# Kernel optimization log

Hardware: AMD Instinct MI355X
Metric: run time of the kernel (lower is better)

The kernel has to match this reference:

```python
import jax, jax.numpy as jnp
import numpy as np

B, N, M = 2, 2048, 128
H, D = 16, 64
IN_DIM, CTX_DIM = 1024, 768


def layernorm(x, g, b, eps=1e-5):
    mu = x.mean(-1, keepdims=True)
    var = ((x - mu) ** 2).mean(-1, keepdims=True)
    return (x - mu) * jax.lax.rsqrt(var + eps) * g + b


def setup_inputs() -> dict:
    key = jax.random.key(0)
    ks = jax.random.split(key, 8)
    w = lambda i, sh: jax.random.normal(ks[i], sh, jnp.float32) * 0.02
    return {
        "x": jax.random.normal(ks[0], (B, N, IN_DIM), jnp.float32),
        "c_emb": jax.random.normal(ks[1], (B, M, CTX_DIM), jnp.float32),
        "ln_g": jnp.ones((IN_DIM,), jnp.float32),
        "ln_b": jnp.zeros((IN_DIM,), jnp.float32),
        "ctx_ln_g": jnp.ones((CTX_DIM,), jnp.float32),
        "ctx_ln_b": jnp.zeros((CTX_DIM,), jnp.float32),
        "W_ctx": w(2, (CTX_DIM, 2 * D)),
        "b_ctx": jnp.zeros((2 * D,), jnp.float32),
        "W_q": w(3, (IN_DIM, H * D)),
        "W_kv": w(4, (IN_DIM, 2 * H * D)),
        "null_kv": jax.random.normal(ks[5], (2, D), jnp.float32),
        "W_out": w(6, (H * D, IN_DIM)),
        "out_ln_g": jnp.ones((IN_DIM,), jnp.float32),
        "out_ln_b": jnp.zeros((IN_DIM,), jnp.float32),
    }


def reference(x, c_emb, ln_g, ln_b, ctx_ln_g, ctx_ln_b, W_ctx, b_ctx,
              W_q, W_kv, null_kv, W_out, out_ln_g, out_ln_b):
    b, n, _ = x.shape
    xn = layernorm(x, ln_g, ln_b)
    q = (xn @ W_q).reshape(b, n, H, D)                      # [b,n,h,d]
    kv = (xn @ W_kv).reshape(b, n, 2, H, D)
    k, v = kv[:, :, 0], kv[:, :, 1]                         # [b,n,h,d]
    # context projected to a single shared-across-heads k and v
    ckv = layernorm(c_emb, ctx_ln_g, ctx_ln_b) @ W_ctx + b_ctx
    ck, cv = jnp.split(ckv, 2, axis=-1)                     # [b,m,d]
    nk = jnp.broadcast_to(null_kv[0], (b, 1, D))
    nv = jnp.broadcast_to(null_kv[1], (b, 1, D))
    k_ext = jnp.concatenate([nk, ck], axis=1)               # [b,m+1,d]
    v_ext = jnp.concatenate([nv, cv], axis=1)
    scale = D ** -0.5
    s_self = jnp.einsum('bnhd,bkhd->bhnk', q, k) * scale    # [b,h,n,n]
    s_ctx = jnp.einsum('bnhd,bkd->bhnk', q, k_ext) * scale  # [b,h,n,m+1]
    w = jax.nn.softmax(jnp.concatenate([s_self, s_ctx], axis=-1), axis=-1)
    w_self, w_ctx = w[..., :n], w[..., n:]
    out = (jnp.einsum('bhnk,bkhd->bnhd', w_self, v)
           + jnp.einsum('bhnk,bkd->bnhd', w_ctx, v_ext))    # [b,n,h,d]
    out = out.reshape(b, n, H * D) @ W_out                  # [b,n,input_dim]
    return layernorm(out, out_ln_g, out_ln_b)
```

## Files before the change

### kernel.cpp

```cpp
#include <hip/hip_runtime.h>
#include <cstdint>
#include <cstddef>

typedef __attribute__((ext_vector_type(8))) short bf16x8;
typedef __attribute__((ext_vector_type(4))) short bf16x4;
typedef __attribute__((ext_vector_type(4))) float f32x4;
typedef __attribute__((ext_vector_type(4))) unsigned int u32x4;
typedef __attribute__((ext_vector_type(2))) unsigned int u32x2;

__device__ inline unsigned short f2b(float f){
  unsigned int u = __float_as_uint(f);
  u += 0x7fffu + ((u >> 16) & 1u);
  return (unsigned short)(u >> 16);
}
__device__ inline unsigned int pk2(float a, float b){
  unsigned int ua = __float_as_uint(a) + 0x8000u;
  unsigned int ub = __float_as_uint(b) + 0x8000u;
  return __builtin_amdgcn_perm(ub, ua, 0x07060302u);
}
__device__ inline void gl2lds16(const void* g, void* l){
  __builtin_amdgcn_global_load_lds(
      (const __attribute__((address_space(1))) unsigned int*)g,
      (__attribute__((address_space(3))) unsigned int*)l, 16, 0, 0);
}

#define QSCALE 0.18033688011112042f

__global__ __launch_bounds__(256) void wcvt_kernel(
    const float* __restrict__ Wq, const float* __restrict__ Wkv,
    const float* __restrict__ Wout,
    unsigned short* __restrict__ Wqkv_t, unsigned short* __restrict__ Wout_t)
{
  __shared__ short tile[64*72];
  int cg0 = blockIdx.x * 64;
  int kt  = blockIdx.y * 64;
  const float* src; int ld; int col0; unsigned short* dst; int drow0;
  if (cg0 < 1024)      { src = Wq;   ld = 1024; col0 = cg0;        dst = Wqkv_t; drow0 = cg0; }
  else if (cg0 < 3072) { src = Wkv;  ld = 2048; col0 = cg0 - 1024; dst = Wqkv_t; drow0 = cg0; }
  else                 { src = Wout; ld = 1024; col0 = cg0 - 3072; dst = Wout_t; drow0 = cg0 - 3072; }
  int t = threadIdx.x;
  #pragma unroll
  for (int i = 0; i < 16; ++i){
    int lin = t + 256*i;
    int k = lin >> 6, c = lin & 63;
    tile[k*72 + c] = (short)f2b(src[(size_t)(kt + k)*ld + col0 + c]);
  }
  __syncthreads();
  #pragma unroll
  for (int i = 0; i < 16; ++i){
    int lin = t + 256*i;
    int c = lin >> 6, k = lin & 63;
    dst[(size_t)(drow0 + c)*1024 + kt + k] = (unsigned short)tile[k*72 + c];
  }
}

template<bool BF16OUT>
__global__ __launch_bounds__(256) void ln1024_kernel(
    const float* __restrict__ X, const float* __restrict__ G,
    const float* __restrict__ Bb, void* __restrict__ out)
{
  int row = blockIdx.x, t = threadIdx.x;
  float4 x = ((const float4*)(X + (size_t)row*1024))[t];
  float s  = x.x + x.y + x.z + x.w;
  float s2 = x.x*x.x + x.y*x.y + x.z*x.z + x.w*x.w;
  #pragma unroll
  for (int o = 32; o > 0; o >>= 1){ s += __shfl_down(s, o); s2 += __shfl_down(s2, o); }
  __shared__ float red[8];
  int w = t >> 6;
  if ((t & 63) == 0){ red[w] = s; red[4 + w] = s2; }
  __syncthreads();
  float mu  = (red[0]+red[1]+red[2]+red[3]) * (1.0f/1024.0f);
  float var = (red[4]+red[5]+red[6]+red[7]) * (1.0f/1024.0f) - mu*mu;
  float rstd = rsqrtf(var + 1e-5f);
  float4 g = ((const float4*)G)[t];
  float4 b = ((const float4*)Bb)[t];
  float y0 = (x.x-mu)*rstd*g.x + b.x;
  float y1 = (x.y-mu)*rstd*g.y + b.y;
  float y2 = (x.z-mu)*rstd*g.z + b.z;
  float y3 = (x.w-mu)*rstd*g.w + b.w;
  if (BF16OUT){
    ushort4 u; u.x = f2b(y0); u.y = f2b(y1); u.z = f2b(y2); u.w = f2b(y3);
    ((ushort4*)out)[(size_t)row*256 + t] = u;
  } else {
    float4 y; y.x = y0; y.y = y1; y.z = y2; y.w = y3;
    ((float4*)out)[(size_t)row*256 + t] = y;
  }
}

__global__ __launch_bounds__(128) void ctx_kernel(
    const float* __restrict__ Cemb, const float* __restrict__ G,
    const float* __restrict__ Bb, const float* __restrict__ Wctx,
    const float* __restrict__ bctx, const float* __restrict__ nullkv,
    unsigned short* __restrict__ kext, unsigned short* __restrict__ vext_t)
{
  int row = blockIdx.x;
  int b = row >> 7, m = row & 127;
  int t = threadIdx.x;
  if (row < 128){
    int b2 = row >> 6, fr = row & 63;
    int frow = (fr == 0) ? 0 : (128 + fr);
    if (t < 64){
      kext[((size_t)b2*192 + frow)*64 + t] = (frow == 0) ? f2b(nullkv[t]) : (unsigned short)0;
    } else {
      int d = t - 64;
      vext_t[((size_t)b2*64 + d)*192 + frow] = (frow == 0) ? f2b(nullkv[64 + d]) : (unsigned short)0;
    }
  }
  const float* xr = Cemb + (size_t)row*768;
  float v[6]; float s = 0.f, s2 = 0.f;
  #pragma unroll
  for (int j = 0; j < 6; ++j){ float xv = xr[t + 128*j]; v[j] = xv; s += xv; s2 += xv*xv; }
  #pragma unroll
  for (int o = 32; o > 0; o >>= 1){ s += __shfl_down(s, o); s2 += __shfl_down(s2, o); }
  __shared__ float red[4];
  __shared__ float xn[768];
  int w = t >> 6;
  if ((t & 63) == 0){ red[w] = s; red[2 + w] = s2; }
  __syncthreads();
  float mu  = (red[0]+red[1]) * (1.0f/768.0f);
  float var = (red[2]+red[3]) * (1.0f/768.0f) - mu*mu;
  float rstd = rsqrtf(var + 1e-5f);
  #pragma unroll
  for (int j = 0; j < 6; ++j){ int c = t + 128*j; xn[c] = (v[j]-mu)*rstd*G[c] + Bb[c]; }
  __syncthreads();
  float acc = bctx[t];
  #pragma unroll 8
  for (int j = 0; j < 768; ++j) acc += xn[j] * Wctx[j*128 + t];
  unsigned short hv = f2b(acc);
  if (t < 64) kext[((size_t)b*192 + 1 + m)*64 + t] = hv;
  else        vext_t[((size_t)b*64 + (t - 64))*192 + 1 + m] = hv;
}

#define GEMM_MAINLOOP(A_, Bt_, tM_, tN_)                                        \
  __shared__ __align__(16) short sA[128*64];                                    \
  __shared__ __align__(16) short sB[128*64];                                    \
  int t = threadIdx.x, w = t >> 6, lane = t & 63;                               \
  int wm = w & 1, wn = w >> 1, lm = lane & 15, q = lane >> 4;                   \
  int grow = lane >> 3;                                                         \
  int gchk = ((lane & 7) ^ grow) << 3;                                          \
  f32x4 acc[4][4] = {};                                                         \
  const unsigned short* Aw = A_ + (size_t)(tM_ + w*32 + grow)*1024 + gchk;      \
  const unsigned short* Bw = Bt_ + (size_t)(tN_ + w*32 + grow)*1024 + gchk;     \
  for (int kk = 0; kk < 1024; kk += 64){                                        \
    __syncthreads();                                                            \
    gl2lds16(Aw + kk,            &sA[(w*32     )*64]);                          \
    gl2lds16(Aw + kk +  8*1024,  &sA[(w*32 +  8)*64]);                          \
    gl2lds16(Aw + kk + 16*1024,  &sA[(w*32 + 16)*64]);                          \
    gl2lds16(Aw + kk + 24*1024,  &sA[(w*32 + 24)*64]);                          \
    gl2lds16(Bw + kk,            &sB[(w*32     )*64]);                          \
    gl2lds16(Bw + kk +  8*1024,  &sB[(w*32 +  8)*64]);                          \
    gl2lds16(Bw + kk + 16*1024,  &sB[(w*32 + 16)*64]);                          \
    gl2lds16(Bw + kk + 24*1024,  &sB[(w*32 + 24)*64]);                          \
    __syncthreads();                                                            \
    bf16x8 af[4][2], bfr[4][2];                                                 \
    _Pragma("unroll")                                                           \
    for (int i = 0; i < 4; ++i){                                                \
      int ra = wm*64 + i*16 + lm, rb = wn*64 + i*16 + lm;                       \
      _Pragma("unroll")                                                         \
      for (int hh = 0; hh < 2; ++hh){                                           \
        int sw = ((hh*4 + q) ^ (lm & 7)) << 3;                                  \
        af[i][hh]  = *(const bf16x8*)(&sA[ra*64 + sw]);                         \
        bfr[i][hh] = *(const bf16x8*)(&sB[rb*64 + sw]);                         \
      }                                                                         \
    }                                                                           \
    _Pragma("unroll")                                                           \
    for (int hh = 0; hh < 2; ++hh)                                              \
      _Pragma("unroll")                                                         \
      for (int i = 0; i < 4; ++i)                                               \
        _Pragma("unroll")                                                       \
        for (int j = 0; j < 4; ++j)                                             \
          acc[i][j] = __builtin_amdgcn_mfma_f32_16x16x32_bf16(af[i][hh], bfr[j][hh], acc[i][j], 0, 0, 0); \
  }

__global__ __launch_bounds__(256) void gemm_qkv_kernel(
    const unsigned short* __restrict__ A, const unsigned short* __restrict__ Bt,
    unsigned short* __restrict__ Qb, unsigned short* __restrict__ Kb,
    unsigned short* __restrict__ VtG)
{
  int id = blockIdx.x;
  int xcd = id & 7, r = id >> 3;
  int tM = ((r & 3)*8 + xcd) * 128;
  int tN = (r >> 2) * 128;
  GEMM_MAINLOOP(A, Bt, tM, tN)
  if (tN < 1024){
    #pragma unroll
    for (int i = 0; i < 4; ++i){
      int R0 = tM + wm*64 + i*16 + q*4;
      int b = R0 >> 11, n = R0 & 2047;
      #pragma unroll
      for (int j = 0; j < 4; ++j){
        int Cg = tN + wn*64 + j*16 + lm;
        int h = Cg >> 6, d = Cg & 63;
        size_t base = ((((size_t)(b*16 + h) << 11) | n) << 6) + d;
        #pragma unroll
        for (int rr = 0; rr < 4; ++rr)
          Qb[base + (size_t)rr*64] = f2b(acc[i][j][rr] * QSCALE);
      }
    }
  } else if (tN < 2048){
    #pragma unroll
    for (int i = 0; i < 4; ++i){
      int R0 = tM + wm*64 + i*16 + q*4;
      int b = R0 >> 11, n = R0 & 2047;
      #pragma unroll
      for (int j = 0; j < 4; ++j){
        int c2 = tN - 1024 + wn*64 + j*16 + lm;
        int h = c2 >> 6, d = c2 & 63;
        size_t base = ((((size_t)(b*16 + h) << 11) | n) << 6) + d;
        #pragma unroll
        for (int rr = 0; rr < 4; ++rr)
          Kb[base + (size_t)rr*64] = f2b(acc[i][j][rr]);
      }
    }
  } else {
    #pragma unroll
    for (int i = 0; i < 4; ++i){
      int R0 = tM + wm*64 + i*16 + q*4;
      int b = R0 >> 11, n = R0 & 2047;
      #pragma unroll
      for (int j = 0; j < 4; ++j){
        int c2 = tN - 2048 + wn*64 + j*16 + lm;
        int h = c2 >> 6, d = c2 & 63;
        ushort4 u;
        u.x = f2b(acc[i][j][0]); u.y = f2b(acc[i][j][1]);
        u.z = f2b(acc[i][j][2]); u.w = f2b(acc[i][j][3]);
        *(ushort4*)(VtG + ((size_t)(b*16 + h)*64 + d)*2048 + n) = u;
      }
    }
  }
}

__global__ __launch_bounds__(256) void gemm_out_kernel(
    const unsigned short* __restrict__ A, const unsigned short* __restrict__ Bt,
    float* __restrict__ C)
{
  int id = blockIdx.x;
  int xcd = id & 7, r = id >> 3;
  int tM = ((r & 3)*8 + xcd) * 128;
  int tN = (r >> 2) * 128;
  GEMM_MAINLOOP(A, Bt, tM, tN)
  #pragma unroll
  for (int i = 0; i < 4; ++i){
    int R0 = tM + wm*64 + i*16 + q*4;
    #pragma unroll
    for (int j = 0; j < 4; ++j){
      int Cg = tN + wn*64 + j*16 + lm;
      #pragma unroll
      for (int rr = 0; rr < 4; ++rr)
        C[(size_t)(R0 + rr)*1024 + Cg] = acc[i][j][rr];
    }
  }
}

__global__ __launch_bounds__(128, 2) void attn_kernel(
    const unsigned short* __restrict__ Qb, const unsigned short* __restrict__ Kb,
    const unsigned short* __restrict__ VtG, const unsigned short* __restrict__ kext,
    const unsigned short* __restrict__ vext_t, unsigned short* __restrict__ Ob)
{
  __shared__ __align__(16) short sK[64*72];
  __shared__ __align__(16) short sVt[64*72];
  __shared__ __align__(16) short sP[2*64*68];
  int id = blockIdx.x;
  int xcd = id & 7, slot = id >> 3;
  int bh = xcd*4 + (slot >> 4);
  int qt = slot & 15;
  int b = bh >> 4, h = bh & 15;
  int t = threadIdx.x, w = t >> 6, lane = t & 63;
  int lm = lane & 15, q = lane >> 4;

  const unsigned short* Qbase = Qb + ((size_t)bh*2048 + qt*128 + w*64)*64;
  bf16x8 qf[4][2];
  #pragma unroll
  for (int qq = 0; qq < 4; ++qq){
    qf[qq][0] = *(const bf16x8*)(Qbase + (size_t)(qq*16 + lm)*64 + q*8);
    qf[qq][1] = *(const bf16x8*)(Qbase + (size_t)(qq*16 + lm)*64 + q*8 + 32);
  }

  f32x4 o[4][4] = {};
  float l_i[4] = {0.f, 0.f, 0.f, 0.f};
  short* pw = &sP[w*64*68];

  int r0 = t >> 1, c0 = (t & 1) << 5;
  u32x4 kr[4], vr[4];
  {
    const unsigned short* kp = Kb + ((size_t)bh*2048 + r0)*64 + c0;
    const unsigned short* vp = VtG + ((size_t)bh*64 + r0)*2048 + c0;
    #pragma unroll
    for (int jj = 0; jj < 4; ++jj){
      kr[jj] = *(const u32x4*)(kp + 8*jj);
      vr[jj] = *(const u32x4*)(vp + 8*jj);
    }
  }

  for (int tile = 0; tile < 35; ++tile){
    __syncthreads();
    #pragma unroll
    for (int jj = 0; jj < 4; ++jj){
      *(u32x4*)(&sK[r0*72 + c0 + 8*jj])  = kr[jj];
      *(u32x4*)(&sVt[r0*72 + c0 + 8*jj]) = vr[jj];
    }
    __syncthreads();

    if (tile + 1 < 35){
      int nt = tile + 1;
      bool ext = nt >= 32;
      int kb = ext ? (nt - 32)*64 : nt*64;
      const unsigned short* kp = ext ? (kext + ((size_t)b*192 + kb + r0)*64 + c0)
                                     : (Kb + ((size_t)bh*2048 + kb + r0)*64 + c0);
      const unsigned short* vp = ext ? (vext_t + ((size_t)b*64 + r0)*192 + kb + c0)
                                     : (VtG + ((size_t)bh*64 + r0)*2048 + kb + c0);
      #pragma unroll
      for (int jj = 0; jj < 4; ++jj){
        kr[jj] = *(const u32x4*)(kp + 8*jj);
        vr[jj] = *(const u32x4*)(vp + 8*jj);
      }
    }

    bf16x8 kf[4][2];
    #pragma unroll
    for (int st = 0; st < 4; ++st){
      kf[st][0] = *(const bf16x8*)(&sK[(st*16 + lm)*72 + q*8]);
      kf[st][1] = *(const bf16x8*)(&sK[(st*16 + lm)*72 + q*8 + 32]);
    }

    #pragma unroll
    for (int qq = 0; qq < 4; ++qq){
      f32x4 s[4];
      #pragma unroll
      for (int st = 0; st < 4; ++st){
        f32x4 z = {};
        z = __builtin_amdgcn_mfma_f32_16x16x32_bf16(kf[st][0], qf[qq][0], z, 0, 0, 0);
        s[st] = __builtin_amdgcn_mfma_f32_16x16x32_bf16(kf[st][1], qf[qq][1], z, 0, 0, 0);
      }
      if (tile == 34){
        #pragma unroll
        for (int st = 0; st < 4; ++st)
          #pragma unroll
          for (int rr = 0; rr < 4; ++rr){
            int key = 128 + st*16 + q*4 + rr;
            if (key >= 129) s[st][rr] = -1e30f;
          }
      }
      float sm = 0.f;
      #pragma unroll
      for (int st = 0; st < 4; ++st)
        #pragma unroll
        for (int rr = 0; rr < 4; ++rr){
          float p = __builtin_amdgcn_exp2f(s[st][rr]);
          s[st][rr] = p; sm += p;
        }
      l_i[qq] += sm;
      #pragma unroll
      for (int st = 0; st < 4; ++st){
        u32x2 pkd;
        pkd[0] = pk2(s[st][0], s[st][1]);
        pkd[1] = pk2(s[st][2], s[st][3]);
        *(u32x2*)(&pw[(qq*16 + lm)*68 + st*16 + q*4]) = pkd;
      }
    }

    bf16x8 pb[4][2];
    #pragma unroll
    for (int qq = 0; qq < 4; ++qq){
      bf16x4 a0 = *(const bf16x4*)(&pw[(qq*16 + lm)*68 + q*8]);
      bf16x4 a1 = *(const bf16x4*)(&pw[(qq*16 + lm)*68 + q*8 + 4]);
      bf16x4 a2 = *(const bf16x4*)(&pw[(qq*16 + lm)*68 + 32 + q*8]);
      bf16x4 a3 = *(const bf16x4*)(&pw[(qq*16 + lm)*68 + 32 + q*8 + 4]);
      pb[qq][0] = __builtin_shufflevector(a0, a1, 0,1,2,3,4,5,6,7);
      pb[qq][1] = __builtin_shufflevector(a2, a3, 0,1,2,3,4,5,6,7);
    }
    #pragma unroll
    for (int ds = 0; ds < 4; ++ds){
      bf16x8 af0 = *(const bf16x8*)(&sVt[(ds*16 + lm)*72 + q*8]);
      bf16x8 af1 = *(const bf16x8*)(&sVt[(ds*16 + lm)*72 + q*8 + 32]);
      #pragma unroll
      for (int qq = 0; qq < 4; ++qq){
        o[ds][qq] = __builtin_amdgcn_mfma_f32_16x16x32_bf16(af0, pb[qq][0], o[ds][qq], 0, 0, 0);
        o[ds][qq] = __builtin_amdgcn_mfma_f32_16x16x32_bf16(af1, pb[qq][1], o[ds][qq], 0, 0, 0);
      }
    }
  }

  #pragma unroll
  for (int qq = 0; qq < 4; ++qq){
    float l = l_i[qq];
    l += __shfl_xor(l, 16);
    l += __shfl_xor(l, 32);
    float inv = 1.0f / l;
    int n = qt*128 + w*64 + qq*16 + lm;
    size_t base = ((size_t)b*2048 + n)*1024 + h*64 + q*4;
    #pragma unroll
    for (int ds = 0; ds < 4; ++ds){
      ushort4 u;
      u.x = f2b(o[ds][qq][0] * inv); u.y = f2b(o[ds][qq][1] * inv);
      u.z = f2b(o[ds][qq][2] * inv); u.w = f2b(o[ds][qq][3] * inv);
      *(ushort4*)(Ob + base + ds*16) = u;
    }
  }
}

extern "C" void kernel_launch(void* const* d_in, const int* in_sizes, int n_in,
                              void* d_out, int out_size, void* d_ws, size_t ws_size,
                              hipStream_t stream)
{
  const float* x       = (const float*)d_in[0];
  const float* c_emb   = (const float*)d_in[1];
  const float* ln_g    = (const float*)d_in[2];
  const float* ln_b    = (const float*)d_in[3];
  const float* ctx_g   = (const float*)d_in[4];
  const float* ctx_b   = (const float*)d_in[5];
  const float* W_ctx   = (const float*)d_in[6];
  const float* b_ctx   = (const float*)d_in[7];
  const float* W_q     = (const float*)d_in[8];
  const float* W_kv    = (const float*)d_in[9];
  const float* null_kv = (const float*)d_in[10];
  const float* W_out   = (const float*)d_in[11];
  const float* oln_g   = (const float*)d_in[12];
  const float* oln_b   = (const float*)d_in[13];
  float* out = (float*)d_out;

  char* p = (char*)d_ws;
  unsigned short* xn     = (unsigned short*)p; p += (size_t)4096*1024*2;
  unsigned short* Wqkv_t = (unsigned short*)p; p += (size_t)3072*1024*2;
  unsigned short* Wout_t = (unsigned short*)p; p += (size_t)1024*1024*2;
  unsigned short* Qb     = (unsigned short*)p; p += (size_t)32*2048*64*2;
  unsigned short* Kb     = (unsigned short*)p; p += (size_t)32*2048*64*2;
  unsigned short* VtG    = (unsigned short*)p; p += (size_t)32*64*2048*2;
  unsigned short* kext   = (unsigned short*)p; p += (size_t)2*192*64*2;
  unsigned short* vext_t = (unsigned short*)p; p += (size_t)2*64*192*2;
  unsigned short* aout   = (unsigned short*)p; p += (size_t)4096*1024*2;
  float*          ptmp   = (float*)p;          p += (size_t)4096*1024*4;

  wcvt_kernel<<<dim3(64,16), 256, 0, stream>>>(W_q, W_kv, W_out, Wqkv_t, Wout_t);
  ln1024_kernel<true><<<4096, 256, 0, stream>>>(x, ln_g, ln_b, (void*)xn);
  ctx_kernel<<<256, 128, 0, stream>>>(c_emb, ctx_g, ctx_b, W_ctx, b_ctx, null_kv, kext, vext_t);
  gemm_qkv_kernel<<<768, 256, 0, stream>>>(xn, Wqkv_t, Qb, Kb, VtG);
  attn_kernel<<<512, 128, 0, stream>>>(Qb, Kb, VtG, kext, vext_t, aout);
  gemm_out_kernel<<<256, 256, 0, stream>>>(aout, Wout_t, ptmp);
  ln1024_kernel<false><<<4096, 256, 0, stream>>>(ptmp, oln_g, oln_b, (void*)out);
}
```

Baseline: 289.1 us.

## Split attention key range across two wave pairs and merge partial outputs

The attention kernel grows from 128 to 256 threads. Two wave pairs each process about half of the 35 key tiles, each with its own K/V shared buffers, and their unnormalized outputs and row sums are merged through shared memory at the end. The QK/PV inner loop is also restructured to handle two query sub-tiles at a time, which lowers live register pressure. This doubles the waves working on each query tile, adding latency hiding, at the cost of a cross-pair reduction, more shared memory per block and uneven 18/17 tile counts between the pairs.

```diff
diff --git a/kernel.cpp b/kernel.cpp
--- a/kernel.cpp
+++ b/kernel.cpp
@@ -252,23 +252,26 @@
   }
 }
 
-__global__ __launch_bounds__(128, 2) void attn_kernel(
+__global__ __launch_bounds__(256, 2) void attn_kernel(
     const unsigned short* __restrict__ Qb, const unsigned short* __restrict__ Kb,
     const unsigned short* __restrict__ VtG, const unsigned short* __restrict__ kext,
     const unsigned short* __restrict__ vext_t, unsigned short* __restrict__ Ob)
 {
-  __shared__ __align__(16) short sK[64*72];
-  __shared__ __align__(16) short sVt[64*72];
-  __shared__ __align__(16) short sP[2*64*68];
+  __shared__ __align__(16) char smem[54272];
   int id = blockIdx.x;
   int xcd = id & 7, slot = id >> 3;
   int bh = xcd*4 + (slot >> 4);
   int qt = slot & 15;
   int b = bh >> 4, h = bh & 15;
   int t = threadIdx.x, w = t >> 6, lane = t & 63;
+  int p = w >> 1, lw = w & 1;
   int lm = lane & 15, q = lane >> 4;
 
-  const unsigned short* Qbase = Qb + ((size_t)bh*2048 + qt*128 + w*64)*64;
+  short* myK = (short*)(smem + p*9216);
+  short* myV = (short*)(smem + 18432 + p*9216);
+  short* pw  = (short*)(smem + 36864 + w*4352);
+
+  const unsigned short* Qbase = Qb + ((size_t)bh*2048 + qt*128 + lw*64)*64;
   bf16x8 qf[4][2];
   #pragma unroll
   for (int qq = 0; qq < 4; ++qq){
@@ -278,13 +281,16 @@
 
   f32x4 o[4][4] = {};
   float l_i[4] = {0.f, 0.f, 0.f, 0.f};
-  short* pw = &sP[w*64*68];
-
-  int r0 = t >> 1, c0 = (t & 1) << 5;
+
+  int pt = t & 127;
+  int r0 = pt >> 1, c0 = (pt & 1) << 5;
+  const int t0 = p ? 18 : 0;
+  const int t1 = p ? 35 : 18;
+
   u32x4 kr[4], vr[4];
   {
-    const unsigned short* kp = Kb + ((size_t)bh*2048 + r0)*64 + c0;
-    const unsigned short* vp = VtG + ((size_t)bh*64 + r0)*2048 + c0;
+    const unsigned short* kp = Kb + ((size_t)bh*2048 + t0*64 + r0)*64 + c0;
+    const unsigned short* vp = VtG + ((size_t)bh*64 + r0)*2048 + t0*64 + c0;
     #pragma unroll
     for (int jj = 0; jj < 4; ++jj){
       kr[jj] = *(const u32x4*)(kp + 8*jj);
@@ -292,17 +298,21 @@
     }
   }
 
-  for (int tile = 0; tile < 35; ++tile){
+  for (int it = 0; it < 18; ++it){
+    int tile = t0 + it;
+    bool valid = tile < t1;
     __syncthreads();
-    #pragma unroll
-    for (int jj = 0; jj < 4; ++jj){
-      *(u32x4*)(&sK[r0*72 + c0 + 8*jj])  = kr[jj];
-      *(u32x4*)(&sVt[r0*72 + c0 + 8*jj]) = vr[jj];
+    if (valid){
+      #pragma unroll
+      for (int jj = 0; jj < 4; ++jj){
+        *(u32x4*)(&myK[r0*72 + c0 + 8*jj]) = kr[jj];
+        *(u32x4*)(&myV[r0*72 + c0 + 8*jj]) = vr[jj];
+      }
     }
     __syncthreads();
 
-    if (tile + 1 < 35){
-      int nt = tile + 1;
+    int nt = tile + 1;
+    if (nt < t1){
       bool ext = nt >= 32;
       int kb = ext ? (nt - 32)*64 : nt*64;
       const unsigned short* kp = ext ? (kext + ((size_t)b*192 + kb + r0)*64 + c0)
@@ -315,86 +325,116 @@
         vr[jj] = *(const u32x4*)(vp + 8*jj);
       }
     }
+    if (!valid) continue;
 
     bf16x8 kf[4][2];
     #pragma unroll
     for (int st = 0; st < 4; ++st){
-      kf[st][0] = *(const bf16x8*)(&sK[(st*16 + lm)*72 + q*8]);
-      kf[st][1] = *(const bf16x8*)(&sK[(st*16 + lm)*72 + q*8 + 32]);
-    }
-
-    #pragma unroll
-    for (int qq = 0; qq < 4; ++qq){
-      f32x4 s[4];
-      #pragma unroll
-      for (int st = 0; st < 4; ++st){
-        f32x4 z = {};
-        z = __builtin_amdgcn_mfma_f32_16x16x32_bf16(kf[st][0], qf[qq][0], z, 0, 0, 0);
-        s[st] = __builtin_amdgcn_mfma_f32_16x16x32_bf16(kf[st][1], qf[qq][1], z, 0, 0, 0);
+      kf[st][0] = *(const bf16x8*)(&myK[(st*16 + lm)*72 + q*8]);
+      kf[st][1] = *(const bf16x8*)(&myK[(st*16 + lm)*72 + q*8 + 32]);
+    }
+
+    #pragma unroll
+    for (int qp = 0; qp < 2; ++qp){
+      f32x4 s[2][4];
+      #pragma unroll
+      for (int qh = 0; qh < 2; ++qh){
+        int qq = qp*2 + qh;
+        #pragma unroll
+        for (int st = 0; st < 4; ++st){
+          f32x4 z = {};
+          z = __builtin_amdgcn_mfma_f32_16x16x32_bf16(kf[st][0], qf[qq][0], z, 0, 0, 0);
+          s[qh][st] = __builtin_amdgcn_mfma_f32_16x16x32_bf16(kf[st][1], qf[qq][1], z, 0, 0, 0);
+        }
       }
       if (tile == 34){
+        #pragma unroll
+        for (int qh = 0; qh < 2; ++qh)
+          #pragma unroll
+          for (int st = 0; st < 4; ++st)
+            #pragma unroll
+            for (int rr = 0; rr < 4; ++rr){
+              int key = 128 + st*16 + q*4 + rr;
+              if (key >= 129) s[qh][st][rr] = -1e30f;
+            }
+      }
+      #pragma unroll
+      for (int qh = 0; qh < 2; ++qh){
+        float sm = 0.f;
         #pragma unroll
         for (int st = 0; st < 4; ++st)
           #pragma unroll
           for (int rr = 0; rr < 4; ++rr){
-            int key = 128 + st*16 + q*4 + rr;
-            if (key >= 129) s[st][rr] = -1e30f;
+            float pv = __builtin_amdgcn_exp2f(s[qh][st][rr]);
+            s[qh][st][rr] = pv; sm += pv;
           }
-      }
-      float sm = 0.f;
-      #pragma unroll
-      for (int st = 0; st < 4; ++st)
-        #pragma unroll
-        for (int rr = 0; rr < 4; ++rr){
-          float p = __builtin_amdgcn_exp2f(s[st][rr]);
-          s[st][rr] = p; sm += p;
+        l_i[qp*2 + qh] += sm;
+        #pragma unroll
+        for (int st = 0; st < 4; ++st){
+          u32x2 pkd;
+          pkd[0] = pk2(s[qh][st][0], s[qh][st][1]);
+          pkd[1] = pk2(s[qh][st][2], s[qh][st][3]);
+          *(u32x2*)(&pw[(qh*16 + lm)*68 + st*16 + q*4]) = pkd;
         }
-      l_i[qq] += sm;
-      #pragma unroll
-      for (int st = 0; st < 4; ++st){
-        u32x2 pkd;
-        pkd[0] = pk2(s[st][0], s[st][1]);
-        pkd[1] = pk2(s[st][2], s[st][3]);
-        *(u32x2*)(&pw[(qq*16 + lm)*68 + st*16 + q*4]) = pkd;
-      }
-    }
-
-    bf16x8 pb[4][2];
+      }
+      bf16x8 pb[2][2];
+      #pragma unroll
+      for (int qh = 0; qh < 2; ++qh){
+        bf16x4 a0 = *(const bf16x4*)(&pw[(qh*16 + lm)*68 + q*8]);
+        bf16x4 a1 = *(const bf16x4*)(&pw[(qh*16 + lm)*68 + q*8 + 4]);
+        bf16x4 a2 = *(const bf16x4*)(&pw[(qh*16 + lm)*68 + 32 + q*8]);
+        bf16x4 a3 = *(const bf16x4*)(&pw[(qh*16 + lm)*68 + 32 + q*8 + 4]);
+        pb[qh][0] = __builtin_shufflevector(a0, a1, 0,1,2,3,4,5,6,7);
+        pb[qh][1] = __builtin_shufflevector(a2, a3, 0,1,2,3,4,5,6,7);
+      }
+      #pragma unroll
+      for (int ds = 0; ds < 4; ++ds){
+        bf16x8 af0 = *(const bf16x8*)(&myV[(ds*16 + lm)*72 + q*8]);
+        bf16x8 af1 = *(const bf16x8*)(&myV[(ds*16 + lm)*72 + q*8 + 32]);
+        #pragma unroll
+        for (int qh = 0; qh < 2; ++qh){
+          int qq = qp*2 + qh;
+          o[ds][qq] = __builtin_amdgcn_mfma_f32_16x16x32_bf16(af0, pb[qh][0], o[ds][qq], 0, 0, 0);
+          o[ds][qq] = __builtin_amdgcn_mfma_f32_16x16x32_bf16(af1, pb[qh][1], o[ds][qq], 0, 0, 0);
+        }
+      }
+    }
+  }
+
+  float* mb = (float*)smem;
+  float* reg = mb + lw*4352 + lane*68;
+  __syncthreads();
+  if (p == 1){
+    #pragma unroll
+    for (int ds = 0; ds < 4; ++ds)
+      #pragma unroll
+      for (int qq = 0; qq < 4; ++qq)
+        *(f32x4*)(reg + (ds*4 + qq)*4) = o[ds][qq];
+    #pragma unroll
+    for (int qq = 0; qq < 4; ++qq) reg[64 + qq] = l_i[qq];
+  }
+  __syncthreads();
+  if (p == 0){
     #pragma unroll
     for (int qq = 0; qq < 4; ++qq){
-      bf16x4 a0 = *(const bf16x4*)(&pw[(qq*16 + lm)*68 + q*8]);
-      bf16x4 a1 = *(const bf16x4*)(&pw[(qq*16 + lm)*68 + q*8 + 4]);
-      bf16x4 a2 = *(const bf16x4*)(&pw[(qq*16 + lm)*68 + 32 + q*8]);
-      bf16x4 a3 = *(const bf16x4*)(&pw[(qq*16 + lm)*68 + 32 + q*8 + 4]);
-      pb[qq][0] = __builtin_shufflevector(a0, a1, 0,1,2,3,4,5,6,7);
-      pb[qq][1] = __builtin_shufflevector(a2, a3, 0,1,2,3,4,5,6,7);
-    }
-    #pragma unroll
-    for (int ds = 0; ds < 4; ++ds){
-      bf16x8 af0 = *(const bf16x8*)(&sVt[(ds*16 + lm)*72 + q*8]);
-      bf16x8 af1 = *(const bf16x8*)(&sVt[(ds*16 + lm)*72 + q*8 + 32]);
-      #pragma unroll
-      for (int qq = 0; qq < 4; ++qq){
-        o[ds][qq] = __builtin_amdgcn_mfma_f32_16x16x32_bf16(af0, pb[qq][0], o[ds][qq], 0, 0, 0);
-        o[ds][qq] = __builtin_amdgcn_mfma_f32_16x16x32_bf16(af1, pb[qq][1], o[ds][qq], 0, 0, 0);
-      }
-    }
-  }
-
-  #pragma unroll
-  for (int qq = 0; qq < 4; ++qq){
-    float l = l_i[qq];
-    l += __shfl_xor(l, 16);
-    l += __shfl_xor(l, 32);
-    float inv = 1.0f / l;
-    int n = qt*128 + w*64 + qq*16 + lm;
-    size_t base = ((size_t)b*2048 + n)*1024 + h*64 + q*4;
-    #pragma unroll
-    for (int ds = 0; ds < 4; ++ds){
-      ushort4 u;
-      u.x = f2b(o[ds][qq][0] * inv); u.y = f2b(o[ds][qq][1] * inv);
-      u.z = f2b(o[ds][qq][2] * inv); u.w = f2b(o[ds][qq][3] * inv);
-      *(ushort4*)(Ob + base + ds*16) = u;
+      #pragma unroll
+      for (int ds = 0; ds < 4; ++ds){
+        f32x4 ov = *(const f32x4*)(reg + (ds*4 + qq)*4);
+        o[ds][qq] += ov;
+      }
+      float l = l_i[qq] + reg[64 + qq];
+      l += __shfl_xor(l, 16);
+      l += __shfl_xor(l, 32);
+      float inv = 1.0f / l;
+      int n = qt*128 + lw*64 + qq*16 + lm;
+      size_t base = ((size_t)b*2048 + n)*1024 + h*64 + q*4;
+      #pragma unroll
+      for (int ds = 0; ds < 4; ++ds){
+        ushort4 u;
+        u.x = f2b(o[ds][qq][0] * inv); u.y = f2b(o[ds][qq][1] * inv);
+        u.z = f2b(o[ds][qq][2] * inv); u.w = f2b(o[ds][qq][3] * inv);
+        *(ushort4*)(Ob + base + ds*16) = u;
+      }
     }
   }
 }
@@ -435,7 +475,7 @@
   ln1024_kernel<true><<<4096, 256, 0, stream>>>(x, ln_g, ln_b, (void*)xn);
   ctx_kernel<<<256, 128, 0, stream>>>(c_emb, ctx_g, ctx_b, W_ctx, b_ctx, null_kv, kext, vext_t);
   gemm_qkv_kernel<<<768, 256, 0, stream>>>(xn, Wqkv_t, Qb, Kb, VtG);
-  attn_kernel<<<512, 128, 0, stream>>>(Qb, Kb, VtG, kext, vext_t, aout);
+  attn_kernel<<<512, 256, 0, stream>>>(Qb, Kb, VtG, kext, vext_t, aout);
   gemm_out_kernel<<<256, 256, 0, stream>>>(aout, Wout_t, ptmp);
   ln1024_kernel<false><<<4096, 256, 0, stream>>>(ptmp, oln_g, oln_b, (void*)out);
 }
```

Result: faster. 273.6 us (-5.4%).

## Split attention KV range across four blocks and merge partials in new kernel

Applied to the files above, without the earlier changes.

Attention is restructured split-KV style: each block now handles 256 queries with 4 waves over one quarter of the 35 key tiles, writing unnormalized bf16 partial outputs and row sums, and a new merge kernel sums the partials and normalizes. K/V tiles are loaded straight into XOR-swizzled LDS with global_load_lds instead of register staging with padding. The QK/softmax/PV work is interleaved per pair of query sub-tiles. The padded-key masking is replaced by subtracting 63 from the merged sum, which relies on exp2 of the zero-padded keys being exactly 1. The extra pass adds partial-output traffic and bf16 rounding of partials, in exchange for more blocks and less per-block latency.

```diff
diff --git a/kernel.cpp b/kernel.cpp
--- a/kernel.cpp
+++ b/kernel.cpp
@@ -252,23 +252,29 @@
   }
 }
 
-__global__ __launch_bounds__(128, 2) void attn_kernel(
+__global__ __launch_bounds__(256, 4) void attn_kernel(
     const unsigned short* __restrict__ Qb, const unsigned short* __restrict__ Kb,
     const unsigned short* __restrict__ VtG, const unsigned short* __restrict__ kext,
-    const unsigned short* __restrict__ vext_t, unsigned short* __restrict__ Ob)
-{
-  __shared__ __align__(16) short sK[64*72];
-  __shared__ __align__(16) short sVt[64*72];
-  __shared__ __align__(16) short sP[2*64*68];
+    const unsigned short* __restrict__ vext_t,
+    unsigned short* __restrict__ Opart, float* __restrict__ Lpart)
+{
+  __shared__ __align__(16) char smem[33792];
+  short* sK  = (short*)smem;
+  short* sVt = (short*)(smem + 8192);
   int id = blockIdx.x;
   int xcd = id & 7, slot = id >> 3;
-  int bh = xcd*4 + (slot >> 4);
-  int qt = slot & 15;
-  int b = bh >> 4, h = bh & 15;
+  int bh = xcd*4 + (slot >> 5);
+  int rem = slot & 31;
+  int qt = rem >> 2, quarter = rem & 3;
+  int b = bh >> 4;
   int t = threadIdx.x, w = t >> 6, lane = t & 63;
   int lm = lane & 15, q = lane >> 4;
-
-  const unsigned short* Qbase = Qb + ((size_t)bh*2048 + qt*128 + w*64)*64;
+  short* pw = (short*)(smem + 16384 + w*4352);
+
+  int grow = lane >> 3;
+  int gchk = ((lane & 7) ^ grow) << 3;
+
+  const unsigned short* Qbase = Qb + ((size_t)bh*2048 + qt*256 + w*64)*64;
   bf16x8 qf[4][2];
   #pragma unroll
   for (int qq = 0; qq < 4; ++qq){
@@ -278,124 +284,141 @@
 
   f32x4 o[4][4] = {};
   float l_i[4] = {0.f, 0.f, 0.f, 0.f};
-  short* pw = &sP[w*64*68];
-
-  int r0 = t >> 1, c0 = (t & 1) << 5;
-  u32x4 kr[4], vr[4];
-  {
-    const unsigned short* kp = Kb + ((size_t)bh*2048 + r0)*64 + c0;
-    const unsigned short* vp = VtG + ((size_t)bh*64 + r0)*2048 + c0;
-    #pragma unroll
-    for (int jj = 0; jj < 4; ++jj){
-      kr[jj] = *(const u32x4*)(kp + 8*jj);
-      vr[jj] = *(const u32x4*)(vp + 8*jj);
-    }
-  }
-
-  for (int tile = 0; tile < 35; ++tile){
+
+  int t0 = quarter*9;
+  for (int it = 0; it < 9; ++it){
+    int tile = t0 + it;
+    bool valid = tile < 35;
     __syncthreads();
-    #pragma unroll
-    for (int jj = 0; jj < 4; ++jj){
-      *(u32x4*)(&sK[r0*72 + c0 + 8*jj])  = kr[jj];
-      *(u32x4*)(&sVt[r0*72 + c0 + 8*jj]) = vr[jj];
+    if (valid){
+      bool ext = tile >= 32;
+      int kb = ext ? (tile - 32)*64 : tile*64;
+      #pragma unroll
+      for (int j = 0; j < 2; ++j){
+        int row = w*16 + j*8 + grow;
+        const unsigned short* kp = ext
+            ? kext + ((size_t)b*192 + kb + row)*64 + gchk
+            : Kb + ((size_t)bh*2048 + kb + row)*64 + gchk;
+        gl2lds16(kp, &sK[(w*16 + j*8)*64]);
+        const unsigned short* vp = ext
+            ? vext_t + ((size_t)b*64 + row)*192 + kb + gchk
+            : VtG + ((size_t)bh*64 + row)*2048 + kb + gchk;
+        gl2lds16(vp, &sVt[(w*16 + j*8)*64]);
+      }
     }
     __syncthreads();
-
-    if (tile + 1 < 35){
-      int nt = tile + 1;
-      bool ext = nt >= 32;
-      int kb = ext ? (nt - 32)*64 : nt*64;
-      const unsigned short* kp = ext ? (kext + ((size_t)b*192 + kb + r0)*64 + c0)
-                                     : (Kb + ((size_t)bh*2048 + kb + r0)*64 + c0);
-      const unsigned short* vp = ext ? (vext_t + ((size_t)b*64 + r0)*192 + kb + c0)
-                                     : (VtG + ((size_t)bh*64 + r0)*2048 + kb + c0);
-      #pragma unroll
-      for (int jj = 0; jj < 4; ++jj){
-        kr[jj] = *(const u32x4*)(kp + 8*jj);
-        vr[jj] = *(const u32x4*)(vp + 8*jj);
-      }
-    }
+    if (!valid) continue;
 
     bf16x8 kf[4][2];
     #pragma unroll
     for (int st = 0; st < 4; ++st){
-      kf[st][0] = *(const bf16x8*)(&sK[(st*16 + lm)*72 + q*8]);
-      kf[st][1] = *(const bf16x8*)(&sK[(st*16 + lm)*72 + q*8 + 32]);
-    }
-
-    #pragma unroll
-    for (int qq = 0; qq < 4; ++qq){
-      f32x4 s[4];
+      int ro = (st*16 + lm)*64, sx = lm & 7;
+      kf[st][0] = *(const bf16x8*)(&sK[ro + ((q ^ sx) << 3)]);
+      kf[st][1] = *(const bf16x8*)(&sK[ro + (((4 + q) ^ sx) << 3)]);
+    }
+
+    #pragma unroll
+    for (int qp = 0; qp < 2; ++qp){
+      float sm0 = 0.f, sm1 = 0.f;
       #pragma unroll
       for (int st = 0; st < 4; ++st){
-        f32x4 z = {};
-        z = __builtin_amdgcn_mfma_f32_16x16x32_bf16(kf[st][0], qf[qq][0], z, 0, 0, 0);
-        s[st] = __builtin_amdgcn_mfma_f32_16x16x32_bf16(kf[st][1], qf[qq][1], z, 0, 0, 0);
-      }
-      if (tile == 34){
+        f32x4 z0 = {}, z1 = {};
+        z0 = __builtin_amdgcn_mfma_f32_16x16x32_bf16(kf[st][0], qf[qp*2  ][0], z0, 0, 0, 0);
+        z0 = __builtin_amdgcn_mfma_f32_16x16x32_bf16(kf[st][1], qf[qp*2  ][1], z0, 0, 0, 0);
+        z1 = __builtin_amdgcn_mfma_f32_16x16x32_bf16(kf[st][0], qf[qp*2+1][0], z1, 0, 0, 0);
+        z1 = __builtin_amdgcn_mfma_f32_16x16x32_bf16(kf[st][1], qf[qp*2+1][1], z1, 0, 0, 0);
+        float p00 = __builtin_amdgcn_exp2f(z0[0]);
+        float p01 = __builtin_amdgcn_exp2f(z0[1]);
+        float p02 = __builtin_amdgcn_exp2f(z0[2]);
+        float p03 = __builtin_amdgcn_exp2f(z0[3]);
+        sm0 += (p00 + p01) + (p02 + p03);
+        u32x2 pk0; pk0[0] = pk2(p00, p01); pk0[1] = pk2(p02, p03);
+        *(u32x2*)(&pw[lm*68 + st*16 + q*4]) = pk0;
+        float p10 = __builtin_amdgcn_exp2f(z1[0]);
+        float p11 = __builtin_amdgcn_exp2f(z1[1]);
+        float p12 = __builtin_amdgcn_exp2f(z1[2]);
+        float p13 = __builtin_amdgcn_exp2f(z1[3]);
+        sm1 += (p10 + p11) + (p12 + p13);
+        u32x2 pk1; pk1[0] = pk2(p10, p11); pk1[1] = pk2(p12, p13);
+        *(u32x2*)(&pw[(16 + lm)*68 + st*16 + q*4]) = pk1;
+      }
+      l_i[qp*2]     += sm0;
+      l_i[qp*2 + 1] += sm1;
+
+      bf16x8 pb[2][2];
+      #pragma unroll
+      for (int qh = 0; qh < 2; ++qh){
+        bf16x4 a0 = *(const bf16x4*)(&pw[(qh*16 + lm)*68 + q*8]);
+        bf16x4 a1 = *(const bf16x4*)(&pw[(qh*16 + lm)*68 + q*8 + 4]);
+        bf16x4 a2 = *(const bf16x4*)(&pw[(qh*16 + lm)*68 + 32 + q*8]);
+        bf16x4 a3 = *(const bf16x4*)(&pw[(qh*16 + lm)*68 + 32 + q*8 + 4]);
+        pb[qh][0] = __builtin_shufflevector(a0, a1, 0,1,2,3,4,5,6,7);
+        pb[qh][1] = __builtin_shufflevector(a2, a3, 0,1,2,3,4,5,6,7);
+      }
+      #pragma unroll
+      for (int ds = 0; ds < 4; ++ds){
+        int ro = (ds*16 + lm)*64, sx = lm & 7;
+        bf16x8 af0 = *(const bf16x8*)(&sVt[ro + ((q ^ sx) << 3)]);
+        bf16x8 af1 = *(const bf16x8*)(&sVt[ro + (((4 + q) ^ sx) << 3)]);
         #pragma unroll
-        for (int st = 0; st < 4; ++st)
-          #pragma unroll
-          for (int rr = 0; rr < 4; ++rr){
-            int key = 128 + st*16 + q*4 + rr;
-            if (key >= 129) s[st][rr] = -1e30f;
-          }
-      }
-      float sm = 0.f;
-      #pragma unroll
-      for (int st = 0; st < 4; ++st)
-        #pragma unroll
-        for (int rr = 0; rr < 4; ++rr){
-          float p = __builtin_amdgcn_exp2f(s[st][rr]);
-          s[st][rr] = p; sm += p;
+        for (int qh = 0; qh < 2; ++qh){
+          int qq = qp*2 + qh;
+          o[ds][qq] = __builtin_amdgcn_mfma_f32_16x16x32_bf16(af0, pb[qh][0], o[ds][qq], 0, 0, 0);
+          o[ds][qq] = __builtin_amdgcn_mfma_f32_16x16x32_bf16(af1, pb[qh][1], o[ds][qq], 0, 0, 0);
         }
-      l_i[qq] += sm;
-      #pragma unroll
-      for (int st = 0; st < 4; ++st){
-        u32x2 pkd;
-        pkd[0] = pk2(s[st][0], s[st][1]);
-        pkd[1] = pk2(s[st][2], s[st][3]);
-        *(u32x2*)(&pw[(qq*16 + lm)*68 + st*16 + q*4]) = pkd;
-      }
-    }
-
-    bf16x8 pb[4][2];
-    #pragma unroll
-    for (int qq = 0; qq < 4; ++qq){
-      bf16x4 a0 = *(const bf16x4*)(&pw[(qq*16 + lm)*68 + q*8]);
-      bf16x4 a1 = *(const bf16x4*)(&pw[(qq*16 + lm)*68 + q*8 + 4]);
-      bf16x4 a2 = *(const bf16x4*)(&pw[(qq*16 + lm)*68 + 32 + q*8]);
-      bf16x4 a3 = *(const bf16x4*)(&pw[(qq*16 + lm)*68 + 32 + q*8 + 4]);
-      pb[qq][0] = __builtin_shufflevector(a0, a1, 0,1,2,3,4,5,6,7);
-      pb[qq][1] = __builtin_shufflevector(a2, a3, 0,1,2,3,4,5,6,7);
-    }
-    #pragma unroll
-    for (int ds = 0; ds < 4; ++ds){
-      bf16x8 af0 = *(const bf16x8*)(&sVt[(ds*16 + lm)*72 + q*8]);
-      bf16x8 af1 = *(const bf16x8*)(&sVt[(ds*16 + lm)*72 + q*8 + 32]);
-      #pragma unroll
-      for (int qq = 0; qq < 4; ++qq){
-        o[ds][qq] = __builtin_amdgcn_mfma_f32_16x16x32_bf16(af0, pb[qq][0], o[ds][qq], 0, 0, 0);
-        o[ds][qq] = __builtin_amdgcn_mfma_f32_16x16x32_bf16(af1, pb[qq][1], o[ds][qq], 0, 0, 0);
-      }
-    }
-  }
-
+      }
+    }
+  }
+
+  int blk = bh*8 + qt;
+  unsigned short* Oph = Opart + ((size_t)blk*4 + quarter)*16384;
+  float* Lph = Lpart + ((size_t)blk*4 + quarter)*256;
   #pragma unroll
   for (int qq = 0; qq < 4; ++qq){
     float l = l_i[qq];
     l += __shfl_xor(l, 16);
     l += __shfl_xor(l, 32);
-    float inv = 1.0f / l;
-    int n = qt*128 + w*64 + qq*16 + lm;
-    size_t base = ((size_t)b*2048 + n)*1024 + h*64 + q*4;
+    int ql = w*64 + qq*16 + lm;
+    if (q == 0) Lph[ql] = l;
     #pragma unroll
     for (int ds = 0; ds < 4; ++ds){
       ushort4 u;
-      u.x = f2b(o[ds][qq][0] * inv); u.y = f2b(o[ds][qq][1] * inv);
-      u.z = f2b(o[ds][qq][2] * inv); u.w = f2b(o[ds][qq][3] * inv);
-      *(ushort4*)(Ob + base + ds*16) = u;
-    }
+      u.x = f2b(o[ds][qq][0]); u.y = f2b(o[ds][qq][1]);
+      u.z = f2b(o[ds][qq][2]); u.w = f2b(o[ds][qq][3]);
+      *(ushort4*)(Oph + ql*64 + ds*16 + q*4) = u;
+    }
+  }
+}
+
+__global__ __launch_bounds__(256) void attn_merge_kernel(
+    const unsigned short* __restrict__ Opart, const float* __restrict__ Lpart,
+    unsigned short* __restrict__ Ob)
+{
+  int blk = blockIdx.x;
+  int bh = blk >> 3, qt = blk & 7;
+  int b = bh >> 4, h = bh & 15;
+  const unsigned short* O0 = Opart + (size_t)blk*4*16384;
+  const float* L0 = Lpart + (size_t)blk*4*256;
+  int t = threadIdx.x;
+  #pragma unroll
+  for (int i = 0; i < 16; ++i){
+    int idx = t + i*256;
+    int ql = idx >> 4, dc = (idx & 15)*4;
+    float l = L0[ql] + L0[256 + ql] + L0[512 + ql] + L0[768 + ql] - 63.0f;
+    float inv = 1.0f / l;
+    float acc0 = 0.f, acc1 = 0.f, acc2 = 0.f, acc3 = 0.f;
+    #pragma unroll
+    for (int qr = 0; qr < 4; ++qr){
+      ushort4 u = *(const ushort4*)(O0 + qr*16384 + idx*4);
+      acc0 += __uint_as_float((unsigned int)u.x << 16);
+      acc1 += __uint_as_float((unsigned int)u.y << 16);
+      acc2 += __uint_as_float((unsigned int)u.z << 16);
+      acc3 += __uint_as_float((unsigned int)u.w << 16);
+    }
+    ushort4 r;
+    r.x = f2b(acc0*inv); r.y = f2b(acc1*inv);
+    r.z = f2b(acc2*inv); r.w = f2b(acc3*inv);
+    *(ushort4*)(Ob + ((size_t)(b*2048 + qt*256 + ql))*1024 + h*64 + dc) = r;
   }
 }
 
@@ -429,13 +452,16 @@
   unsigned short* kext   = (unsigned short*)p; p += (size_t)2*192*64*2;
   unsigned short* vext_t = (unsigned short*)p; p += (size_t)2*64*192*2;
   unsigned short* aout   = (unsigned short*)p; p += (size_t)4096*1024*2;
-  float*          ptmp   = (float*)p;          p += (size_t)4096*1024*4;
+  unsigned short* Opart  = (unsigned short*)p; p += (size_t)4*4096*1024*2;
+  float*          Lpart  = (float*)p;          p += (size_t)256*4*256*4;
+  float*          ptmp   = (float*)Opart;
 
   wcvt_kernel<<<dim3(64,16), 256, 0, stream>>>(W_q, W_kv, W_out, Wqkv_t, Wout_t);
   ln1024_kernel<true><<<4096, 256, 0, stream>>>(x, ln_g, ln_b, (void*)xn);
   ctx_kernel<<<256, 128, 0, stream>>>(c_emb, ctx_g, ctx_b, W_ctx, b_ctx, null_kv, kext, vext_t);
   gemm_qkv_kernel<<<768, 256, 0, stream>>>(xn, Wqkv_t, Qb, Kb, VtG);
-  attn_kernel<<<512, 128, 0, stream>>>(Qb, Kb, VtG, kext, vext_t, aout);
+  attn_kernel<<<1024, 256, 0, stream>>>(Qb, Kb, VtG, kext, vext_t, Opart, Lpart);
+  attn_merge_kernel<<<256, 256, 0, stream>>>(Opart, Lpart, aout);
   gemm_out_kernel<<<256, 256, 0, stream>>>(aout, Wout_t, ptmp);
   ln1024_kernel<false><<<4096, 256, 0, stream>>>(ptmp, oln_g, oln_b, (void*)out);
 }
```

Measured after the change: 430.1 us. +48.8%, slower.
